# Performance work log

Measured on AMD Instinct MI355X. Metric: run time of the kernel, lower is better.

The kernel has to match this reference:

```python
import jax, jax.numpy as jnp
import numpy as np

N_QUBITS = 12
LAYERS = 2
BATCH = 1024


def _apply_1q(state, gate, q):
    # state: [B] + [2]*n (wire 0 = leading qubit axis); gate: [2,2] or [B,2,2]
    axis = 1 + q
    st = jnp.moveaxis(state, axis, -1)
    if gate.ndim == 2:
        st = jnp.einsum('ij,...j->...i', gate, st)
    else:  # batched gate (angle depends on the input sample)
        st = jnp.einsum('bij,b...j->b...i', gate, st)
    return jnp.moveaxis(st, -1, axis)


def _apply_cnot(state, c, t):
    # flip target axis on the control=1 slice
    ca, ta = 1 + c, 1 + t
    a0 = jnp.take(state, 0, axis=ca)
    a1 = jnp.take(state, 1, axis=ca)
    ta2 = ta - 1 if ta > ca else ta
    a1 = jnp.flip(a1, axis=ta2)
    return jnp.stack([a0, a1], axis=ca)


def _rx(a):
    # a: [B] -> gate [B,2,2]
    h = 0.5 * a
    c = jnp.cos(h).astype(jnp.complex64)
    s = (-1j) * jnp.sin(h).astype(jnp.complex64)
    return jnp.stack([jnp.stack([c, s], -1), jnp.stack([s, c], -1)], -2)


def _ry(a):
    h = 0.5 * a
    c = jnp.cos(h).astype(jnp.complex64)
    s = jnp.sin(h).astype(jnp.complex64)
    return jnp.stack([jnp.stack([c, -s], -1), jnp.stack([s, c], -1)], -2)


def _rz(a):
    h = 0.5 * a
    e0 = jnp.exp(-1j * h.astype(jnp.complex64))
    e1 = jnp.exp(1j * h.astype(jnp.complex64))
    z = jnp.zeros_like(e0)
    return jnp.stack([jnp.stack([e0, z], -1), jnp.stack([z, e1], -1)], -2)


def setup_inputs() -> dict:
    key = jax.random.key(0)
    k1, k2 = jax.random.split(key)
    x = jax.random.normal(k1, (BATCH, N_QUBITS), dtype=jnp.float32)
    theta = jax.random.normal(k2, (LAYERS, N_QUBITS, 2), dtype=jnp.float32)
    lam = jnp.ones((LAYERS, N_QUBITS), dtype=jnp.float32)
    return {"x": x, "theta": theta, "lam": lam}


def reference(x, theta, lam):
    B = x.shape[0]
    n = N_QUBITS
    # |0...0> state, batched: [B] + [2]*n
    state = jnp.zeros((B,) + (2,) * n, dtype=jnp.complex64)
    state = state.at[(slice(None),) + (0,) * n].set(1.0)
    for l in range(LAYERS):
        for q in range(n):
            state = _apply_1q(state, _rx(lam[l, q] * x[:, q]), q)
        for q in range(n):
            state = _apply_cnot(state, q, (q + 1) % n)
        for q in range(n):
            state = _apply_1q(state, _ry(theta[l, q, 0]), q)
            state = _apply_1q(state, _rz(theta[l, q, 1]), q)
    probs = state.real ** 2 + state.imag ** 2  # [B] + [2]*n
    zs = []
    for q in range(n):
        axes = tuple(i for i in range(1, n + 1) if i != 1 + q)
        p = jnp.sum(probs, axis=axes)  # [B, 2]
        zs.append(p[:, 0] - p[:, 1])   # <Z_q>
    return jnp.stack(zs, axis=1)  # [B, n_qubits]
```

## Files before the change

### kernel.cpp

```cpp
#include <hip/hip_runtime.h>
#include <math.h>

#define NQ 12
#define TPB 256


__device__ __forceinline__ void g_fused(float2& a0, float2& a1,
                                        float cy, float sy, float cz, float sz)
{
    float n0x = cy*a0.x - sy*a1.x;
    float n0y = cy*a0.y - sy*a1.y;
    float wx  = sy*a0.x + cy*a1.x;
    float wy  = sy*a0.y + cy*a1.y;
    a0.x = n0x; a0.y = n0y;
    a1.x = cz*wx - sz*wy;
    a1.y = cz*wy + sz*wx;
}

__device__ __forceinline__ void g_rx(float2& a0, float2& a1, float c, float s)
{
    float n0x = c*a0.x + s*a1.y;
    float n0y = c*a0.y - s*a1.x;
    float n1x = c*a1.x + s*a0.y;
    float n1y = c*a1.y - s*a0.x;
    a0.x = n0x; a0.y = n0y; a1.x = n1x; a1.y = n1y;
}

__device__ __forceinline__ void g_ry(float2& a0, float2& a1, float c, float s)
{
    float n0x = c*a0.x - s*a1.x;
    float n0y = c*a0.y - s*a1.y;
    float n1x = s*a0.x + c*a1.x;
    float n1y = s*a0.y + c*a1.y;
    a0.x = n0x; a0.y = n0y; a1.x = n1x; a1.y = n1y;
}

#define FOR_PAIRS4(RB, STMT) do {                                     \
    const int msk_ = 1 << (RB);                                       \
    _Pragma("unroll")                                                 \
    for (int h_ = 0; h_ < 8; ++h_) {                                  \
        const int i0 = ((h_ & ~(msk_ - 1)) << 1) | (h_ & (msk_ - 1)); \
        const int i1 = i0 | msk_;                                     \
        STMT;                                                         \
    } } while (0)

#define ADDR_A(r) (((r) << 8) | (t & 0xF0) | ((t ^ (t >> 4) ^ (r)) & 15))
#define ADDR_B(r) (((t >> 4) << 8) | ((r) << 4) | ((t ^ (r) ^ (t >> 4)) & 15))
#define ADDR_C(r) ((t << 4) | (((r) ^ t ^ (t >> 4)) & 15))


__global__ __launch_bounds__(TPB) void vqc_kernel(
    const float* __restrict__ x,
    const float* __restrict__ th,
    const float* __restrict__ lm,
    float* __restrict__ out)
{
    __shared__ float2 S[4096];
    __shared__ float2 co[60];

    const int b = blockIdx.x;
    const int t = threadIdx.x;
    const int l = t & 63;
    const int w = t >> 6;

    if (t < 60) {
        float h;
        if (t < 12)       h = 0.5f * lm[t] * x[b * NQ + t];
        else if (t < 24)  h = 0.5f * lm[t] * x[b * NQ + (t - 12)];
        else if (t < 36)  h = 0.5f * th[2 * (t - 24)];
        else if (t < 48)  h = th[2 * (t - 36) + 1];
        else              h = 0.5f * th[24 + 2 * (t - 48)];
        float c, s;
        __sincosf(h, &s, &c);
        co[t].x = c; co[t].y = s;
    }
    __syncthreads();

    float2 v[16];

    {
        const int g = (t ^ (t >> 1)) & 0x7F;
        float Pt = 1.0f;
#pragma unroll
        for (int p = 0; p < 7; ++p) {
            float2 cs = co[11 - p];
            Pt *= ((g >> p) & 1) ? cs.y : cs.x;
        }
        const int ct = __popc(g);
        const int n7 = (t >> 7) & 1, n0 = t & 1;
        float2 cs4 = co[4], cs3 = co[3], cs2 = co[2], cs1 = co[1], cs0 = co[0];
        const float a7  = n7 ? cs4.y : cs4.x;
        const float a7x = n7 ? cs4.x : cs4.y;
        const float a10 = n0 ? cs1.y : cs1.x;
        const float a10x= n0 ? cs1.x : cs1.y;
        const float a11 = n0 ? cs0.y : cs0.x;
        const float a11x= n0 ? cs0.x : cs0.y;
        float F89[4];
        F89[0] = cs3.x * cs2.x; F89[1] = cs3.x * cs2.y;
        F89[2] = cs3.y * cs2.x; F89[3] = cs3.y * cs2.y;

#pragma unroll
        for (int r = 0; r < 16; ++r) {
            const int r0 = r & 1, r1 = (r >> 1) & 1, r2 = (r >> 2) & 1,
                      r3 = r >> 3;
            const int i8 = r0 ^ r1, i9 = r1 ^ r2;
            float m = Pt * (r0 ? a7x : a7) * F89[(i8 << 1) | i9]
            int k = (ct + (n7 ^ r0) + i8 + i9 + (n0 ^ r2 ^ r3) + (n0 ^ r3)) & 3;
            v[r].x = (k == 0) ? m : ((k == 2) ? -m : 0.0f);
            v[r].y = (k == 3) ? m : ((k == 1) ? -m : 0.0f);
        }
    }

#define G_GATE(q, RB) do {                                                \
        float2 csy = co[24 + (q)];                                        \
        float2 csz = co[36 + (q)];                                        \
        FOR_PAIRS4(RB, g_fused(v[i0], v[i1], csy.x, csy.y, csz.x, csz.y));\
    } while (0)

#pragma unroll
    for (int q = 0; q < 4; ++q) G_GATE(q, 3 - q);

#pragma unroll
    for (int r = 0; r < 16; ++r) S[ADDR_A(r)] = v[r];
    __syncthreads();
#pragma unroll
    for (int r = 0; r < 16; ++r) v[r] = S[ADDR_B(r)];
    __syncthreads();

#pragma unroll
    for (int q = 4; q < 8; ++q) G_GATE(q, 7 - q);

#pragma unroll
    for (int r = 0; r < 16; ++r) S[ADDR_B(r)] = v[r];
    __syncthreads();
#pragma unroll
    for (int r = 0; r < 16; ++r) v[r] = S[ADDR_C(r)];
    __syncthreads();

#pragma unroll
    for (int q = 8; q < 12; ++q) G_GATE(q, 11 - q);

#define RX_GATE(q, RB) do {                                               \
        float2 cs = co[12 + (q)];                                         \
        FOR_PAIRS4(RB, g_rx(v[i0], v[i1], cs.x, cs.y));                   \
    } while (0)

#pragma unroll
    for (int q = 8; q < 12; ++q) RX_GATE(q, 11 - q);

#pragma unroll
    for (int r = 0; r < 16; ++r) S[ADDR_C(r)] = v[r];
    __syncthreads();
#pragma unroll
    for (int r = 0; r < 16; ++r) v[r] = S[ADDR_B(r)];
    __syncthreads();

#pragma unroll
    for (int q = 4; q < 8; ++q) RX_GATE(q, 7 - q);

#pragma unroll
    for (int r = 0; r < 16; ++r) S[ADDR_B(r)] = v[r];
    __syncthreads();
#pragma unroll
    for (int r = 0; r < 16; ++r) v[r] = S[ADDR_A(r)];
    __syncthreads();

#pragma unroll
    for (int q = 0; q < 4; ++q) RX_GATE(q, 3 - q);

#pragma unroll
    for (int r = 0; r < 16; ++r) {
        int j = (r << 8) | t;
        int y = j ^ (j >> 1); y ^= y >> 2; y ^= y >> 4; y ^= y >> 8;
        int p = (y & 0x7FF) | (((__popc(j) ^ (j >> 11)) & 1) << 11);
        int ad = (p & ~15) | ((p ^ (p >> 4) ^ (p >> 8)) & 15);
        S[ad] = v[r];
    }
    __syncthreads();
#pragma unroll
    for (int r = 0; r < 16; ++r) v[r] = S[ADDR_C(r)];
    __syncthreads();

#define RY_GATE(q, RB) do {                                               \
        float2 cs = co[48 + (q)];                                         \
        FOR_PAIRS4(RB, g_ry(v[i0], v[i1], cs.x, cs.y));                   \
    } while (0)

#pragma unroll
    for (int q = 8; q < 12; ++q) RY_GATE(q, 11 - q);

#pragma unroll
    for (int r = 0; r < 16; ++r) S[ADDR_C(r)] = v[r];
    __syncthreads();
#pragma unroll
    for (int r = 0; r < 16; ++r) v[r] = S[ADDR_B(r)];
    __syncthreads();

#pragma unroll
    for (int q = 4; q < 8; ++q) RY_GATE(q, 7 - q);

#pragma unroll
    for (int r = 0; r < 16; ++r) S[ADDR_B(r)] = v[r];
    __syncthreads();
#pragma unroll
    for (int r = 0; r < 16; ++r) v[r] = S[ADDR_A(r)];
    __syncthreads();

#pragma unroll
    for (int q = 0; q < 4; ++q) RY_GATE(q, 3 - q);

    float ptot = 0.0f;
    float zb[4] = {0.f, 0.f, 0.f, 0.f};
#pragma unroll
    for (int r = 0; r < 16; ++r) {
        float p = v[r].x * v[r].x + v[r].y * v[r].y;
        ptot += p;
#pragma unroll
        for (int q = 0; q < 4; ++q)
            zb[q] += ((r >> (3 - q)) & 1) ? -p : p;
    }
    float tv[NQ];
#pragma unroll
    for (int q = 0; q < 4; ++q) tv[q] = zb[q];
#pragma unroll
    for (int q = 4; q < 12; ++q)
        tv[q] = ((t >> (11 - q)) & 1) ? -ptot : ptot;

#pragma unroll
    for (int q = 0; q < NQ; ++q) {
#pragma unroll
        for (int m = 1; m < 64; m <<= 1)
            tv[q] += __shfl_xor(tv[q], m, 64);
    }

    float* red = (float*)S;
    if (l == 0) {
#pragma unroll
        for (int q = 0; q < NQ; ++q) red[w * NQ + q] = tv[q];
    }
    __syncthreads();
    if (t < NQ)
        out[b * NQ + t] = red[t] + red[NQ + t] + red[2 * NQ + t] + red[3 * NQ + t];
}

extern "C" void kernel_launch(void* const* d_in, const int* in_sizes, int n_in,
                              void* d_out, int out_size, void* d_ws, size_t ws_size,
                              hipStream_t stream) {
    const int B = in_sizes[0] / NQ;
    vqc_kernel<<<B, TPB, 0, stream>>>((const float*)d_in[0],
                                      (const float*)d_in[1],
                                      (const float*)d_in[2],
                                      (float*)d_out);
}
```

Baseline: 87.74 us.

## Split state across 512 threads with 8 amplitudes each and 3-qubit phases

Doubles the threads per block from 256 to 512, so each thread holds 8 amplitudes instead of 16 and applies gates in groups of 3 qubits. This needs four register/shared-memory transposes per sweep instead of three, each followed by block-wide barriers. The aim is more parallelism and lower register pressure per thread, at the cost of extra barriers and shared-memory traffic. The final reduction now sums over 8 waves.

```diff
diff --git a/kernel.cpp b/kernel.cpp
--- a/kernel.cpp
+++ b/kernel.cpp
@@ -2,8 +2,12 @@
 #include <math.h>
 
 #define NQ 12
-#define TPB 256
-
+#define TPB 512
+
+
+__device__ __forceinline__ int phys(int j) {
+    return (j & ~15) | ((j ^ (j >> 4) ^ (j >> 8)) & 15);
+}
 
 __device__ __forceinline__ void g_fused(float2& a0, float2& a1,
                                         float cy, float sy, float cz, float sz)
@@ -35,19 +39,48 @@
     a0.x = n0x; a0.y = n0y; a1.x = n1x; a1.y = n1y;
 }
 
-#define FOR_PAIRS4(RB, STMT) do {                                     \
+#define FOR_PAIRS3(RB, STMT) do {                                     \
     const int msk_ = 1 << (RB);                                       \
     _Pragma("unroll")                                                 \
-    for (int h_ = 0; h_ < 8; ++h_) {                                  \
+    for (int h_ = 0; h_ < 4; ++h_) {                                  \
         const int i0 = ((h_ & ~(msk_ - 1)) << 1) | (h_ & (msk_ - 1)); \
         const int i1 = i0 | msk_;                                     \
         STMT;                                                         \
     } } while (0)
 
-#define ADDR_A(r) (((r) << 8) | (t & 0xF0) | ((t ^ (t >> 4) ^ (r)) & 15))
-#define ADDR_B(r) (((t >> 4) << 8) | ((r) << 4) | ((t ^ (r) ^ (t >> 4)) & 15))
-#define ADDR_C(r) ((t << 4) | (((r) ^ t ^ (t >> 4)) & 15))
-
+#define J_A(r) (((r) << 9) | t)
+#define J_B(r) (((t >> 6) << 9) | ((r) << 6) | (t & 63))
+#define J_C(r) (((t >> 3) << 6) | ((r) << 3) | (t & 7))
+#define J_D(r) ((t << 3) | (r))
+
+#define XPOSE(JSRC, JDST) do {                                        \
+    _Pragma("unroll")                                                 \
+    for (int r_ = 0; r_ < 8; ++r_) S[phys(JSRC(r_))] = v[r_];         \
+    __syncthreads();                                                  \
+    _Pragma("unroll")                                                 \
+    for (int r_ = 0; r_ < 8; ++r_) v[r_] = S[phys(JDST(r_))];         \
+    __syncthreads();                                                  \
+  } while (0)
+
+#define G_PHASE(QB) do { _Pragma("unroll")                                  \
+    for (int d_ = 0; d_ < 3; ++d_) {                                        \
+        float2 csy = co[24 + (QB) + d_];                                    \
+        float2 csz = co[36 + (QB) + d_];                                    \
+        FOR_PAIRS3(2 - d_, g_fused(v[i0], v[i1], csy.x, csy.y,              \
+                                   csz.x, csz.y));                          \
+    } } while (0)
+
+#define RX_PHASE(QB) do { _Pragma("unroll")                                 \
+    for (int d_ = 0; d_ < 3; ++d_) {                                        \
+        float2 cs = co[12 + (QB) + d_];                                     \
+        FOR_PAIRS3(2 - d_, g_rx(v[i0], v[i1], cs.x, cs.y));                 \
+    } } while (0)
+
+#define RY_PHASE(QB) do { _Pragma("unroll")                                 \
+    for (int d_ = 0; d_ < 3; ++d_) {                                        \
+        float2 cs = co[48 + (QB) + d_];                                     \
+        FOR_PAIRS3(2 - d_, g_ry(v[i0], v[i1], cs.x, cs.y));                 \
+    } } while (0)
 
 __global__ __launch_bounds__(TPB) void vqc_kernel(
     const float* __restrict__ x,
@@ -76,154 +109,88 @@
     }
     __syncthreads();
 
-    float2 v[16];
+    float2 v[8];
 
     {
-        const int g = (t ^ (t >> 1)) & 0x7F;
+        const int g = (t ^ (t >> 1)) & 0xFF;
         float Pt = 1.0f;
 #pragma unroll
-        for (int p = 0; p < 7; ++p) {
+        for (int p = 0; p < 8; ++p) {
             float2 cs = co[11 - p];
             Pt *= ((g >> p) & 1) ? cs.y : cs.x;
         }
         const int ct = __popc(g);
-        const int n7 = (t >> 7) & 1, n0 = t & 1;
-        float2 cs4 = co[4], cs3 = co[3], cs2 = co[2], cs1 = co[1], cs0 = co[0];
-        const float a7  = n7 ? cs4.y : cs4.x;
-        const float a7x = n7 ? cs4.x : cs4.y;
-        const float a10 = n0 ? cs1.y : cs1.x;
-        const float a10x= n0 ? cs1.x : cs1.y;
-        const float a11 = n0 ? cs0.y : cs0.x;
-        const float a11x= n0 ? cs0.x : cs0.y;
-        float F89[4];
-        F89[0] = cs3.x * cs2.x; F89[1] = cs3.x * cs2.y;
-        F89[2] = cs3.y * cs2.x; F89[3] = cs3.y * cs2.y;
-
-#pragma unroll
-        for (int r = 0; r < 16; ++r) {
-            const int r0 = r & 1, r1 = (r >> 1) & 1, r2 = (r >> 2) & 1,
-                      r3 = r >> 3;
-            const int i8 = r0 ^ r1, i9 = r1 ^ r2;
-            float m = Pt * (r0 ? a7x : a7) * F89[(i8 << 1) | i9]
-            int k = (ct + (n7 ^ r0) + i8 + i9 + (n0 ^ r2 ^ r3) + (n0 ^ r3)) & 3;
+        const int t8 = (t >> 8) & 1, t0 = t & 1;
+        float2 q3 = co[3], q2 = co[2], q1 = co[1], q0 = co[0];
+        const float u3  = t8 ? q3.y : q3.x;
+        const float u3n = t8 ? q3.x : q3.y;
+        const float u1  = t0 ? q1.y : q1.x;
+        const float u1n = t0 ? q1.x : q1.y;
+        const float u0  = t0 ? q0.y : q0.x;
+        const float u0n = t0 ? q0.x : q0.y;
+#pragma unroll
+        for (int r = 0; r < 8; ++r) {
+            const int r0 = r & 1, r1 = (r >> 1) & 1, r2 = (r >> 2) & 1;
+            const int i9 = r0 ^ r1;
+            float m = Pt * (r0 ? u3n : u3) * (i9 ? q2.y : q2.x)
+                         * ((r1 ^ r2) ? u1n : u1) * (r2 ? u0n : u0);
+            int k = (ct + (t8 ^ r0) + i9 + (t0 ^ r1 ^ r2) + (t0 ^ r2)) & 3;
             v[r].x = (k == 0) ? m : ((k == 2) ? -m : 0.0f);
             v[r].y = (k == 3) ? m : ((k == 1) ? -m : 0.0f);
         }
     }
 
-#define G_GATE(q, RB) do {                                                \
-        float2 csy = co[24 + (q)];                                        \
-        float2 csz = co[36 + (q)];                                        \
-        FOR_PAIRS4(RB, g_fused(v[i0], v[i1], csy.x, csy.y, csz.x, csz.y));\
-    } while (0)
-
-#pragma unroll
-    for (int q = 0; q < 4; ++q) G_GATE(q, 3 - q);
-
-#pragma unroll
-    for (int r = 0; r < 16; ++r) S[ADDR_A(r)] = v[r];
-    __syncthreads();
-#pragma unroll
-    for (int r = 0; r < 16; ++r) v[r] = S[ADDR_B(r)];
-    __syncthreads();
-
-#pragma unroll
-    for (int q = 4; q < 8; ++q) G_GATE(q, 7 - q);
-
-#pragma unroll
-    for (int r = 0; r < 16; ++r) S[ADDR_B(r)] = v[r];
-    __syncthreads();
-#pragma unroll
-    for (int r = 0; r < 16; ++r) v[r] = S[ADDR_C(r)];
-    __syncthreads();
-
-#pragma unroll
-    for (int q = 8; q < 12; ++q) G_GATE(q, 11 - q);
-
-#define RX_GATE(q, RB) do {                                               \
-        float2 cs = co[12 + (q)];                                         \
-        FOR_PAIRS4(RB, g_rx(v[i0], v[i1], cs.x, cs.y));                   \
-    } while (0)
-
-#pragma unroll
-    for (int q = 8; q < 12; ++q) RX_GATE(q, 11 - q);
-
-#pragma unroll
-    for (int r = 0; r < 16; ++r) S[ADDR_C(r)] = v[r];
-    __syncthreads();
-#pragma unroll
-    for (int r = 0; r < 16; ++r) v[r] = S[ADDR_B(r)];
-    __syncthreads();
-
-#pragma unroll
-    for (int q = 4; q < 8; ++q) RX_GATE(q, 7 - q);
-
-#pragma unroll
-    for (int r = 0; r < 16; ++r) S[ADDR_B(r)] = v[r];
-    __syncthreads();
-#pragma unroll
-    for (int r = 0; r < 16; ++r) v[r] = S[ADDR_A(r)];
-    __syncthreads();
-
-#pragma unroll
-    for (int q = 0; q < 4; ++q) RX_GATE(q, 3 - q);
-
-#pragma unroll
-    for (int r = 0; r < 16; ++r) {
-        int j = (r << 8) | t;
+    G_PHASE(0);
+    XPOSE(J_A, J_B);
+    G_PHASE(3);
+    XPOSE(J_B, J_C);
+    G_PHASE(6);
+    XPOSE(J_C, J_D);
+    G_PHASE(9);
+
+    RX_PHASE(9);
+    XPOSE(J_D, J_C);
+    RX_PHASE(6);
+    XPOSE(J_C, J_B);
+    RX_PHASE(3);
+    XPOSE(J_B, J_A);
+    RX_PHASE(0);
+
+#pragma unroll
+    for (int r = 0; r < 8; ++r) {
+        int j = J_A(r);
         int y = j ^ (j >> 1); y ^= y >> 2; y ^= y >> 4; y ^= y >> 8;
         int p = (y & 0x7FF) | (((__popc(j) ^ (j >> 11)) & 1) << 11);
-        int ad = (p & ~15) | ((p ^ (p >> 4) ^ (p >> 8)) & 15);
-        S[ad] = v[r];
-    }
-    __syncthreads();
-#pragma unroll
-    for (int r = 0; r < 16; ++r) v[r] = S[ADDR_C(r)];
-    __syncthreads();
-
-#define RY_GATE(q, RB) do {                                               \
-        float2 cs = co[48 + (q)];                                         \
-        FOR_PAIRS4(RB, g_ry(v[i0], v[i1], cs.x, cs.y));                   \
-    } while (0)
-
-#pragma unroll
-    for (int q = 8; q < 12; ++q) RY_GATE(q, 11 - q);
-
-#pragma unroll
-    for (int r = 0; r < 16; ++r) S[ADDR_C(r)] = v[r];
-    __syncthreads();
-#pragma unroll
-    for (int r = 0; r < 16; ++r) v[r] = S[ADDR_B(r)];
-    __syncthreads();
-
-#pragma unroll
-    for (int q = 4; q < 8; ++q) RY_GATE(q, 7 - q);
-
-#pragma unroll
-    for (int r = 0; r < 16; ++r) S[ADDR_B(r)] = v[r];
-    __syncthreads();
-#pragma unroll
-    for (int r = 0; r < 16; ++r) v[r] = S[ADDR_A(r)];
-    __syncthreads();
-
-#pragma unroll
-    for (int q = 0; q < 4; ++q) RY_GATE(q, 3 - q);
+        S[phys(p)] = v[r];
+    }
+    __syncthreads();
+#pragma unroll
+    for (int r = 0; r < 8; ++r) v[r] = S[phys(J_D(r))];
+    __syncthreads();
+
+    RY_PHASE(9);
+    XPOSE(J_D, J_C);
+    RY_PHASE(6);
+    XPOSE(J_C, J_B);
+    RY_PHASE(3);
+    XPOSE(J_B, J_A);
+    RY_PHASE(0);
 
     float ptot = 0.0f;
-    float zb[4] = {0.f, 0.f, 0.f, 0.f};
-#pragma unroll
-    for (int r = 0; r < 16; ++r) {
+    float zb[3] = {0.f, 0.f, 0.f};
+#pragma unroll
+    for (int r = 0; r < 8; ++r) {
         float p = v[r].x * v[r].x + v[r].y * v[r].y;
         ptot += p;
 #pragma unroll
-        for (int q = 0; q < 4; ++q)
-            zb[q] += ((r >> (3 - q)) & 1) ? -p : p;
+        for (int q = 0; q < 3; ++q)
+            zb[q] += ((r >> (2 - q)) & 1) ? -p : p;
     }
     float tv[NQ];
 #pragma unroll
-    for (int q = 0; q < 4; ++q) tv[q] = zb[q];
-#pragma unroll
-    for (int q = 4; q < 12; ++q)
+    for (int q = 0; q < 3; ++q) tv[q] = zb[q];
+#pragma unroll
+    for (int q = 3; q < 12; ++q)
         tv[q] = ((t >> (11 - q)) & 1) ? -ptot : ptot;
 
 #pragma unroll
@@ -239,8 +206,12 @@
         for (int q = 0; q < NQ; ++q) red[w * NQ + q] = tv[q];
     }
     __syncthreads();
-    if (t < NQ)
-        out[b * NQ + t] = red[t] + red[NQ + t] + red[2 * NQ + t] + red[3 * NQ + t];
+    if (t < NQ) {
+        float r = 0.f;
+#pragma unroll
+        for (int ww = 0; ww < 8; ++ww) r += red[ww * NQ + t];
+        out[b * NQ + t] = r;
+    }
 }
 
 extern "C" void kernel_launch(void* const* d_in, const int* in_sizes, int n_in,
```

New measurement: 91.98 us. 1.05x slower.
